# Optimization experiments

Measured on AMD Instinct MI355X. Metric: run time of the kernel, lower is better.

Reference implementation:

```python
import jax, jax.numpy as jnp
import numpy as np
from jax import lax

B, C_IN, H, W = 16, 2048, 16, 16
HIDDEN, N_ANC = 512, 9
N_POS, N_NEG = 2048, 2048
TOT = B * N_ANC * H * W  # 36864 = flat conf logits; also rows of reg.view(-1,4)


def _xyxy_to_cxcywh(b):
    x1, y1, x2, y2 = b[..., 0], b[..., 1], b[..., 2], b[..., 3]
    return jnp.stack([(x1 + x2) * 0.5, (y1 + y2) * 0.5, x2 - x1, y2 - y1], axis=-1)


def _cxcywh_to_xyxy(b):
    cx, cy, w, h = b[..., 0], b[..., 1], b[..., 2], b[..., 3]
    return jnp.stack([cx - w * 0.5, cy - h * 0.5, cx + w * 0.5, cy + h * 0.5], axis=-1)


def _rand_boxes(key, n):
    # valid xyxy boxes on the 16x16 feature-map coordinate grid, w,h in [1,4]
    k1, k2 = jax.random.split(key)
    xy = jax.random.uniform(k1, (n, 2), jnp.float32) * 12.0
    wh = 1.0 + jax.random.uniform(k2, (n, 2), jnp.float32) * 3.0
    return jnp.concatenate([xy, xy + wh], axis=-1)


def setup_inputs() -> dict:
    key = jax.random.key(0)
    ks = jax.random.split(key, 10)
    feature_map = jax.random.normal(ks[0], (B, C_IN, H, W), jnp.float32)
    pos_anc_ind = jax.random.randint(ks[1], (N_POS,), 0, TOT)
    neg_anc_ind = jax.random.randint(ks[2], (N_NEG,), 0, TOT)
    pos_anc_coords = _rand_boxes(ks[3], N_POS)
    gt_bboxes_pos = _rand_boxes(ks[4], N_POS)
    s1 = 1.0 / np.sqrt(C_IN * 9)
    W1 = jax.random.uniform(ks[5], (HIDDEN, C_IN, 3, 3), jnp.float32, -s1, s1)
    b1 = jnp.zeros((HIDDEN,), jnp.float32)
    s2 = 1.0 / np.sqrt(HIDDEN)
    Wc = jax.random.uniform(ks[6], (N_ANC, HIDDEN), jnp.float32, -s2, s2)
    bc = jnp.zeros((N_ANC,), jnp.float32)
    Wr = jax.random.uniform(ks[7], (N_ANC * 4, HIDDEN), jnp.float32, -s2, s2)
    br = jnp.zeros((N_ANC * 4,), jnp.float32)
    return {"feature_map": feature_map, "pos_anc_coords": pos_anc_coords,
            "gt_bboxes_pos": gt_bboxes_pos, "W1": W1, "b1": b1, "Wc": Wc,
            "bc": bc, "Wr": Wr, "br": br,
            "pos_anc_ind": pos_anc_ind, "neg_anc_ind": neg_anc_ind}


def generate_proposals(anchors, offsets):
    a = _xyxy_to_cxcywh(anchors)
    p = jnp.stack([a[:, 0] + offsets[:, 0] * a[:, 2],
                   a[:, 1] + offsets[:, 1] * a[:, 3],
                   a[:, 2] * jnp.exp(offsets[:, 2]),
                   a[:, 3] * jnp.exp(offsets[:, 3])], axis=-1)
    return _cxcywh_to_xyxy(p)


def calc_gt_offsets(anc, gt):
    a = _xyxy_to_cxcywh(anc)
    g = _xyxy_to_cxcywh(gt)
    tx = (g[:, 0] - a[:, 0]) / a[:, 2]
    ty = (g[:, 1] - a[:, 1]) / a[:, 3]
    tw = jnp.log(g[:, 2] / a[:, 2])
    th = jnp.log(g[:, 3] / a[:, 3])
    return jnp.stack([tx, ty, tw, th], axis=-1)


def reference(feature_map, pos_anc_coords, gt_bboxes_pos, W1, b1, Wc, bc, Wr, br,
              pos_anc_ind, neg_anc_ind):
    # ProposalModule: conv3x3 -> (dropout=identity in eval) -> relu -> 1x1 heads
    out = lax.conv_general_dilated(feature_map, W1, (1, 1), 'SAME',
                                   dimension_numbers=('NCHW', 'OIHW', 'NCHW'))
    out = jax.nn.relu(out + b1[None, :, None, None])
    conf = jnp.einsum('bchw,oc->bohw', out, Wc) + bc[None, :, None, None]   # [B,9,H,W]
    reg = jnp.einsum('bchw,oc->bohw', out, Wr) + br[None, :, None, None]    # [B,36,H,W]
    # irregular flat gathers, exactly mirroring torch .flatten()/.view(-1,4)
    conf_pos = conf.reshape(-1)[pos_anc_ind]
    conf_neg = conf.reshape(-1)[neg_anc_ind]
    offsets_pos = reg.reshape(-1, 4)[pos_anc_ind]
    proposals = generate_proposals(pos_anc_coords, offsets_pos)
    gt_offsets = calc_gt_offsets(pos_anc_coords, gt_bboxes_pos)
    # BCE-with-logits, targets 1 for pos / 0 for neg, reduction='sum' / B
    cls_loss = (jnp.sum(jax.nn.softplus(-conf_pos)) + jnp.sum(jax.nn.softplus(conf_neg))) / B
    # smooth L1 (beta=1), reduction='sum' / B
    d = offsets_pos - gt_offsets
    ad = jnp.abs(d)
    reg_loss = jnp.sum(jnp.where(ad < 1.0, 0.5 * d * d, ad - 0.5)) / B
    total_rpn_loss = 1.0 * cls_loss + 5.0 * reg_loss  # w_conf=1, w_reg=5
    return total_rpn_loss, proposals
```

## Files before the change

kernel.cpp:

```cpp
#include <hip/hip_runtime.h>
#include <hip/hip_bf16.h>
#include <stdint.h>

#define CIN 2048
#define HID 512
#define NPOS 2048
#define NNEG 2048

#define BM 256
#define BN 256
#define BK 64
#define NS 8
#define A_ELEMS (BM * BK)
#define B_ELEMS (BN * BK)

typedef __attribute__((ext_vector_type(8))) short s16x8;
typedef __attribute__((ext_vector_type(4))) short s16x4;
typedef __attribute__((ext_vector_type(4))) float f32x4;
typedef unsigned short ushort_t;

static __device__ __forceinline__ float bf2f(unsigned short u) {
    union { float f; unsigned int i; } v; v.i = ((unsigned int)u) << 16; return v.f;
}
static __device__ __forceinline__ unsigned short f2bf(float f) {
    union { float f; unsigned int i; } v; v.f = f;
    unsigned int r = v.i + 0x7FFF + ((v.i >> 16) & 1);
    return (unsigned short)(r >> 16);
}

typedef __attribute__((address_space(1))) const void gvoid_t;
typedef __attribute__((address_space(3))) void lvoid_t;
static __device__ __forceinline__ void gload16(const void* g, void* l) {
    __builtin_amdgcn_global_load_lds((gvoid_t*)g, (lvoid_t*)l, 16, 0, 0);
}

__global__ __launch_bounds__(256) void k_prep(const float* __restrict__ F,
                                              const float* __restrict__ W1,
                                              const float* __restrict__ Wc,
                                              const float* __restrict__ Wr,
                                              ushort_t* __restrict__ Fp,
                                              ushort_t* __restrict__ Wt2,
                                              ushort_t* __restrict__ Whp) {
    __shared__ float tile[128][17];
    __shared__ float buf[512 * 9];
    int bid = blockIdx.x;
    int t = threadIdx.x;
    if (bid < 1024) {
        int b = bid >> 6, rem = bid & 63;
        int y = rem >> 2, icq = rem & 3;
        for (int it = 0; it < 4; ++it) {
            int ic0 = icq * 512 + it * 128;
#pragma unroll
            for (int i2 = 0; i2 < 2; ++i2) {
                int idx = i2 * 256 + t;
                int ci = idx >> 2, xg = idx & 3;
                const float4 v = *(const float4*)&F[((size_t)(b * CIN + ic0 + ci) * 16 + y) * 16 + xg * 4];
                tile[ci][xg * 4 + 0] = v.x;
                tile[ci][xg * 4 + 1] = v.y;
                tile[ci][xg * 4 + 2] = v.z;
                tile[ci][xg * 4 + 3] = v.w;
            }
            __syncthreads();
#pragma unroll
            for (int i2 = 0; i2 < 2; ++i2) {
                int idx = i2 * 256 + t;
                int x = idx >> 5, cig = idx & 31;
                s16x4 o;
#pragma unroll
                for (int j = 0; j < 4; ++j) o[j] = (short)f2bf(tile[cig * 4 + j][x]);
                *(s16x4*)&Fp[((size_t)(b * 18 + y + 1) * 18 + (x + 1)) * CIN + ic0 + cig * 4] = o;
            }
            __syncthreads();
        }
    } else if (bid < 1536) {
        int oc = bid - 1024;
        for (int ic0 = 0; ic0 < CIN; ic0 += 512) {
            const float* src = W1 + ((size_t)oc * CIN + ic0) * 9;
            {
                const float4* s4 = (const float4*)src;
                float4* b4 = (float4*)buf;
                for (int i = t; i < 1152; i += 256) b4[i] = s4[i];
            }
            __syncthreads();
            for (int s = t; s < 9 * 64; s += 256) {
                int k = s >> 6, g = s & 63;
                s16x8 v;
#pragma unroll
                for (int j = 0; j < 8; ++j) v[j] = (short)f2bf(buf[(g * 8 + j) * 9 + k]);
                *(s16x8*)&Wt2[((size_t)(k * HID + oc)) * CIN + ic0 + g * 8] = v;
            }
            __syncthreads();
        }
    } else if (bid < 1600) {
        const s16x8 z = {0, 0, 0, 0, 0, 0, 0, 0};
        for (int idx = (bid - 1536) * 256 + t; idx < 16 * 68 * 256; idx += 64 * 256) {
            int seg = idx & 255;
            int cell = (idx >> 8) % 68;
            int b = idx / (68 * 256);
            int Y, X;
            if (cell < 18)      { Y = 0;         X = cell; }
            else if (cell < 36) { Y = 17;        X = cell - 18; }
            else if (cell < 52) { Y = cell - 35; X = 0; }
            else                { Y = cell - 51; X = 17; }
            *(s16x8*)&Fp[((size_t)(b * 18 + Y) * 18 + X) * CIN + seg * 8] = z;
        }
    } else {
#pragma unroll
        for (int i = 0; i < 12; ++i) {
            int sid = i * 256 + t;
            int o = sid >> 6, sg = sid & 63;
            s16x8 v;
#pragma unroll
            for (int j = 0; j < 8; ++j) {
                float w = 0.f;
                if (o < 9) w = Wc[o * HID + sg * 8 + j];
                else if (o < 45) w = Wr[(size_t)(o - 9) * HID + sg * 8 + j];
                v[j] = (short)f2bf(w);
            }
            *(s16x8*)&Whp[o * HID + ((sg ^ (o & 7)) << 3)] = v;
        }
    }
}

__global__ __launch_bounds__(512, 2) void k_gemm(const ushort_t* __restrict__ Fp,
                                                 const ushort_t* __restrict__ Wt2,
                                                 ushort_t* __restrict__ Part,
                                                 int icLen, int nPairs) {
    extern __shared__ ushort_t ldsbuf[];
    ushort_t* As = ldsbuf;
    ushort_t* Bs = ldsbuf + 3 * A_ELEMS;

    int bid = blockIdx.x;
    int rb = bid / nPairs;
    int pair = bid - rb * nPairs;
    int split = pair >> 1, cb = pair & 1;
    int icBase = split * icLen;
    int m0 = rb * BM, oc0 = cb * BN;
    int t = threadIdx.x;
    int wid = t >> 6, lane = t & 63;
    int wr = wid >> 2, wn = wid & 3;
    int hi = lane >> 4, lo = lane & 15;

    f32x4 acc[8][4];
#pragma unroll
    for (int a = 0; a < 8; ++a)
#pragma unroll
        for (int b = 0; b < 4; ++b) acc[a][b] = (f32x4){0.f, 0.f, 0.f, 0.f};

    int Abase[4], Bbase[4];
#pragma unroll
    for (int j = 0; j < 4; ++j) {
        int li = j * 512 + t;
        int row = li >> 3;
        int sg = (li & 7) ^ (row & 7);
        int m = m0 + row;
        int b = m >> 8, y = (m >> 4) & 15, x = m & 15;
        Abase[j] = ((b * 18 + y) * 18 + x) * CIN + sg * 8;
        Bbase[j] = (oc0 + row) * CIN + sg * 8;
    }
    int aidx[8][2], bidx[4][2];
#pragma unroll
    for (int fm = 0; fm < 8; ++fm)
#pragma unroll
        for (int ks = 0; ks < 2; ++ks) {
            int r = wr * 128 + fm * 16 + lo;
            aidx[fm][ks] = r * BK + ((ks * 32 + hi * 8) ^ ((r & 7) << 3));
        }
#pragma unroll
    for (int fn = 0; fn < 4; ++fn)
#pragma unroll
        for (int ks = 0; ks < 2; ++ks) {
            int rB = wn * 64 + fn * 16 + lo;
            bidx[fn][ks] = rB * BK + ((ks * 32 + hi * 8) ^ ((rB & 7) << 3));
        }

    const int nsteps = (icLen / BK) * 9;

#define STAGE_A(BUF, S)                                                              \
    do {                                                                             \
        int kidx_ = (S) % 9, icc_ = (S) / 9;                                         \
        int ak_ = ((kidx_ / 3) * 18 + (kidx_ - 3 * (kidx_ / 3))) * CIN + icBase + icc_ * BK; \
        ushort_t* dA_ = As + (BUF) * A_ELEMS;                                        \
        _Pragma("unroll") for (int j_ = 0; j_ < 4; ++j_)                             \
            gload16(Fp + Abase[j_] + ak_, dA_ + (size_t)(j_ * 512 + t) * 8);         \
    } while (0)
#define STAGE_B(BUF, S)                                                              \
    do {                                                                             \
        int kidx_ = (S) % 9, icc_ = (S) / 9;                                         \
        int bk_ = kidx_ * HID * CIN + icBase + icc_ * BK;                            \
        ushort_t* dB_ = Bs + (BUF) * B_ELEMS;                                        \
        _Pragma("unroll") for (int j_ = 0; j_ < 4; ++j_)                             \
            gload16(Wt2 + Bbase[j_] + bk_, dB_ + (size_t)(j_ * 512 + t) * 8);        \
    } while (0)

    STAGE_A(0, 0); STAGE_B(0, 0); STAGE_A(1, 1);
    asm volatile("s_waitcnt vmcnt(4)" ::: "memory");
    __builtin_amdgcn_s_barrier();
    __builtin_amdgcn_sched_barrier(0);

#pragma unroll 1
    for (int step = 0; step < nsteps; ++step) {
        const ushort_t* cA = As + (step % 3) * A_ELEMS;
        const ushort_t* cB = Bs + (step & 1) * B_ELEMS;
        if (step + 1 < nsteps) STAGE_B((step + 1) & 1, step + 1);
        s16x8 af[8][2], bf[4][2];
#pragma unroll
        for (int ks = 0; ks < 2; ++ks) {
#pragma unroll
            for (int fm = 0; fm < 8; ++fm) af[fm][ks] = *(const s16x8*)&cA[aidx[fm][ks]];
#pragma unroll
            for (int fn = 0; fn < 4; ++fn) bf[fn][ks] = *(const s16x8*)&cB[bidx[fn][ks]];
        }
        if (step + 2 < nsteps) STAGE_A((step + 2) % 3, step + 2);
        __builtin_amdgcn_s_setprio(1);
#pragma unroll
        for (int fm = 0; fm < 8; ++fm)
#pragma unroll
            for (int fn = 0; fn < 4; ++fn)
#pragma unroll
                for (int ks = 0; ks < 2; ++ks)
                    acc[fm][fn] = __builtin_amdgcn_mfma_f32_16x16x32_bf16(
                        af[fm][ks], bf[fn][ks], acc[fm][fn], 0, 0, 0);
        __builtin_amdgcn_s_setprio(0);
        if (step + 2 < nsteps) {
            asm volatile("s_waitcnt vmcnt(4)" ::: "memory");
            __builtin_amdgcn_s_barrier();
            __builtin_amdgcn_sched_barrier(0);
        } else if (step + 1 < nsteps) {
            asm volatile("s_waitcnt vmcnt(0)" ::: "memory");
            __builtin_amdgcn_s_barrier();
            __builtin_amdgcn_sched_barrier(0);
        }
    }
#undef STAGE_A
#undef STAGE_B

#pragma unroll
    for (int fm = 0; fm < 8; ++fm)
#pragma unroll
        for (int fn = 0; fn < 4; ++fn)
#pragma unroll
            for (int r = 0; r < 4; ++r) {
                int gm = m0 + wr * 128 + fm * 16 + hi * 4 + r;
                int gn = oc0 + wn * 64 + fn * 16 + lo;
                Part[((size_t)split * 4096 + gm) * HID + gn] = f2bf(acc[fm][fn][r]);
            }
}

__global__ __launch_bounds__(256) void k_heads(const ushort_t* __restrict__ Part, int ns,
                                               const ushort_t* __restrict__ Whp,
                                               const float* __restrict__ b1,
                                               const float* __restrict__ bc,
                                               const float* __restrict__ br,
                                               float* __restrict__ conf,
                                               float* __restrict__ reg) {
    extern __shared__ ushort_t hsm[];
    ushort_t* Ah = hsm;
    ushort_t* Wh = hsm + 16 * HID;
    int t = threadIdx.x;
    int wid = t >> 6, lane = t & 63;
    int hi = lane >> 4, lo = lane & 15;
    int row0 = blockIdx.x * 16;

#pragma unroll
    for (int i = 0; i < 12; ++i)
        gload16(Whp + (size_t)(i * 256 + t) * 8, Wh + (size_t)(i * 256 + t) * 8);

#pragma unroll
    for (int i = 0; i < 4; ++i) {
        int pos = i * 256 + t;
        int r = pos >> 6, sg = pos & 63;
        float s[8];
#pragma unroll
        for (int j = 0; j < 8; ++j) s[j] = 0.f;
        for (int sp = 0; sp < ns; ++sp) {
            s16x8 v = *(const s16x8*)&Part[((size_t)sp * 4096 + row0 + r) * HID + sg * 8];
#pragma unroll
            for (int j = 0; j < 8; ++j) s[j] += bf2f((unsigned short)v[j]);
        }
        s16x8 o;
#pragma unroll
        for (int j = 0; j < 8; ++j) o[j] = (short)f2bf(fmaxf(s[j] + b1[sg * 8 + j], 0.f));
        *(s16x8*)&Ah[r * HID + ((sg ^ (r & 7)) << 3)] = o;
    }
    __syncthreads();
    if (wid != 0) return;

    f32x4 acc[3];
#pragma unroll
    for (int fn = 0; fn < 3; ++fn) acc[fn] = (f32x4){0.f, 0.f, 0.f, 0.f};
#pragma unroll 1
    for (int kf = 0; kf < 16; ++kf) {
        int rA = lo;
        s16x8 a_ = *(const s16x8*)&Ah[rA * HID + ((kf * 32 + hi * 8) ^ ((rA & 7) << 3))];
#pragma unroll
        for (int fn = 0; fn < 3; ++fn) {
            int rB = fn * 16 + lo;
            s16x8 b_ = *(const s16x8*)&Wh[rB * HID + ((kf * 32 + hi * 8) ^ ((rB & 7) << 3))];
            acc[fn] = __builtin_amdgcn_mfma_f32_16x16x32_bf16(a_, b_, acc[fn], 0, 0, 0);
        }
    }
#pragma unroll
    for (int fn = 0; fn < 3; ++fn)
#pragma unroll
        for (int r = 0; r < 4; ++r) {
            int gm = row0 + hi * 4 + r;
            int o = fn * 16 + lo;
            float v = acc[fn][r];
            if (o < 9) conf[gm * 9 + o] = v + bc[o];
            else if (o < 45) reg[gm * 36 + (o - 9)] = v + br[o - 9];
        }
}

static __device__ __forceinline__ float softplus(float x) {
    return log1pf(expf(-fabsf(x))) + fmaxf(x, 0.f);
}

__global__ __launch_bounds__(1024) void k_loss(const float* __restrict__ conf,
                                               const float* __restrict__ reg,
                                               const int* __restrict__ pos_ind,
                                               const int* __restrict__ neg_ind,
                                               const float* __restrict__ anc,
                                               const float* __restrict__ gt,
                                               float* __restrict__ out) {
    int t = threadIdx.x;
    float cls = 0.f, rloss = 0.f;
    for (int p = t; p < NPOS; p += 1024) {
        int ind = pos_ind[p];
        {
            int b = ind / 2304, r = ind % 2304;
            int c = r >> 8, r2 = r & 255;
            float cv = conf[(b * 256 + r2) * 9 + c];
            cls += softplus(-cv);
        }
        float off[4];
#pragma unroll
        for (int j = 0; j < 4; ++j) {
            int e = 4 * ind + j;
            int b = e / 9216, r = e % 9216;
            int c = r >> 8, r2 = r & 255;
            off[j] = reg[(b * 256 + r2) * 36 + c];
        }
        float ax1 = anc[4 * p], ay1 = anc[4 * p + 1], ax2 = anc[4 * p + 2], ay2 = anc[4 * p + 3];
        float acx = (ax1 + ax2) * 0.5f, acy = (ay1 + ay2) * 0.5f;
        float aw = ax2 - ax1, ah = ay2 - ay1;
        float pcx = acx + off[0] * aw, pcy = acy + off[1] * ah;
        float pw = aw * expf(off[2]), ph = ah * expf(off[3]);
        out[1 + 4 * p + 0] = pcx - pw * 0.5f;
        out[1 + 4 * p + 1] = pcy - ph * 0.5f;
        out[1 + 4 * p + 2] = pcx + pw * 0.5f;
        out[1 + 4 * p + 3] = pcy + ph * 0.5f;
        float gx1 = gt[4 * p], gy1 = gt[4 * p + 1], gx2 = gt[4 * p + 2], gy2 = gt[4 * p + 3];
        float gcx = (gx1 + gx2) * 0.5f, gcy = (gy1 + gy2) * 0.5f;
        float gw = gx2 - gx1, gh = gy2 - gy1;
        float tv[4];
        tv[0] = (gcx - acx) / aw;
        tv[1] = (gcy - acy) / ah;
        tv[2] = logf(gw / aw);
        tv[3] = logf(gh / ah);
#pragma unroll
        for (int j = 0; j < 4; ++j) {
            float d = off[j] - tv[j];
            float ad = fabsf(d);
            rloss += (ad < 1.f) ? 0.5f * d * d : ad - 0.5f;
        }
    }
    for (int q = t; q < NNEG; q += 1024) {
        int ind = neg_ind[q];
        int b = ind / 2304, r = ind % 2304;
        int c = r >> 8, r2 = r & 255;
        float cv = conf[(b * 256 + r2) * 9 + c];
        cls += softplus(cv);
    }
    __shared__ float s1[1024], s2[1024];
    s1[t] = cls;
    s2[t] = rloss;
    __syncthreads();
    for (int s = 512; s > 0; s >>= 1) {
        if (t < s) {
            s1[t] += s1[t + s];
            s2[t] += s2[t + s];
        }
        __syncthreads();
    }
    if (t == 0) out[0] = (s1[0] + 5.f * s2[0]) / 16.f;
}

extern "C" void kernel_launch(void* const* d_in, const int* in_sizes, int n_in,
                              void* d_out, int out_size, void* d_ws, size_t ws_size,
                              hipStream_t stream) {
    const float* F   = (const float*)d_in[0];
    const float* anc = (const float*)d_in[1];
    const float* gt  = (const float*)d_in[2];
    const float* W1  = (const float*)d_in[3];
    const float* b1  = (const float*)d_in[4];
    const float* Wc  = (const float*)d_in[5];
    const float* bc  = (const float*)d_in[6];
    const float* Wr  = (const float*)d_in[7];
    const float* br  = (const float*)d_in[8];
    const int* pos_ind = (const int*)d_in[9];
    const int* neg_ind = (const int*)d_in[10];
    float* out = (float*)d_out;

    char* ws = (char*)d_ws;
    const size_t FP_BYTES   = (size_t)16 * 18 * 18 * CIN * 2;
    const size_t WT_BYTES   = (size_t)9 * HID * CIN * 2;
    const size_t PART_ONE   = (size_t)4096 * HID * 2;
    const size_t CONF_BYTES = (size_t)4096 * 9 * 4;
    const size_t REG_BYTES  = (size_t)4096 * 36 * 4;

    int icLen = CIN / NS;

    ushort_t* Fp   = (ushort_t*)ws;
    ushort_t* Wt2  = (ushort_t*)(ws + FP_BYTES);
    ushort_t* Part = (ushort_t*)(ws + FP_BYTES + WT_BYTES);
    float* conf    = (float*)(ws + FP_BYTES + WT_BYTES + (size_t)NS * PART_ONE);
    float* reg     = (float*)(ws + FP_BYTES + WT_BYTES + (size_t)NS * PART_ONE + CONF_BYTES);
    ushort_t* Whp  = (ushort_t*)(ws + FP_BYTES + WT_BYTES + (size_t)NS * PART_ONE + CONF_BYTES + REG_BYTES);

    const int GEMM_LDS = (3 * A_ELEMS + 2 * B_ELEMS) * 2;
    hipFuncSetAttribute((const void*)k_gemm, hipFuncAttributeMaxDynamicSharedMemorySize, GEMM_LDS);
    const int HEADS_LDS = (16 + 48) * HID * 2;
    hipFuncSetAttribute((const void*)k_heads, hipFuncAttributeMaxDynamicSharedMemorySize, HEADS_LDS);

    k_prep<<<1601, 256, 0, stream>>>(F, W1, Wc, Wr, Fp, Wt2, Whp);
    k_gemm<<<(4096 / BM) * (HID / BN) * NS, 512, GEMM_LDS, stream>>>(Fp, Wt2, Part, icLen, 2 * NS);
    k_heads<<<256, 256, HEADS_LDS, stream>>>(Part, NS, Whp, b1, bc, br, conf, reg);
    k_loss<<<1, 1024, 0, stream>>>(conf, reg, pos_ind, neg_ind, anc, gt, out);
}
```

Measured before the change: 125.4 us.

## Halve GEMM K-tile and register double-buffer LDS fragments in a ping-pong loop

The K tile of the implicit-GEMM conv drops from 64 to 32. LDS changes from 3 A buffers plus 2 B buffers to 2 of each, shrinking from 160KB to 64KB, and the swizzle is adjusted for the 4-segment rows. The main loop is rebuilt as a two-stage ping-pong: fragments for the next buffer are read into registers while the MFMAs run on the current ones, with one combined A+B stage per step and a full vmcnt/lgkmcnt(0) wait plus barrier after each step. This is meant to overlap LDS reads with MFMA work, but it doubles the number of barriers per unit of K, removes the partial vmcnt overlap the old code had, and raises register pressure by holding two fragment sets.

Result: slower. 132.7 us (+5.8%).

```diff
diff --git a/kernel.cpp b/kernel.cpp
--- a/kernel.cpp
+++ b/kernel.cpp
@@ -9,7 +9,7 @@
 
 #define BM 256
 #define BN 256
-#define BK 64
+#define BK 32
 #define NS 8
 #define A_ELEMS (BM * BK)
 #define B_ELEMS (BN * BK)
@@ -128,7 +128,7 @@
                                                  int icLen, int nPairs) {
     extern __shared__ ushort_t ldsbuf[];
     ushort_t* As = ldsbuf;
-    ushort_t* Bs = ldsbuf + 3 * A_ELEMS;
+    ushort_t* Bs = ldsbuf + 2 * A_ELEMS;
 
     int bid = blockIdx.x;
     int rb = bid / nPairs;
@@ -147,93 +147,92 @@
 #pragma unroll
         for (int b = 0; b < 4; ++b) acc[a][b] = (f32x4){0.f, 0.f, 0.f, 0.f};
 
-    int Abase[4], Bbase[4];
-#pragma unroll
-    for (int j = 0; j < 4; ++j) {
+    int Abase[2], Bbase[2];
+#pragma unroll
+    for (int j = 0; j < 2; ++j) {
         int li = j * 512 + t;
-        int row = li >> 3;
-        int sg = (li & 7) ^ (row & 7);
+        int row = li >> 2;
+        int sg = (li & 3) ^ ((row >> 1) & 3);
         int m = m0 + row;
         int b = m >> 8, y = (m >> 4) & 15, x = m & 15;
         Abase[j] = ((b * 18 + y) * 18 + x) * CIN + sg * 8;
         Bbase[j] = (oc0 + row) * CIN + sg * 8;
     }
-    int aidx[8][2], bidx[4][2];
-#pragma unroll
-    for (int fm = 0; fm < 8; ++fm)
-#pragma unroll
-        for (int ks = 0; ks < 2; ++ks) {
-            int r = wr * 128 + fm * 16 + lo;
-            aidx[fm][ks] = r * BK + ((ks * 32 + hi * 8) ^ ((r & 7) << 3));
-        }
-#pragma unroll
-    for (int fn = 0; fn < 4; ++fn)
-#pragma unroll
-        for (int ks = 0; ks < 2; ++ks) {
-            int rB = wn * 64 + fn * 16 + lo;
-            bidx[fn][ks] = rB * BK + ((ks * 32 + hi * 8) ^ ((rB & 7) << 3));
-        }
+    int aidx[8], bidx[4];
+#pragma unroll
+    for (int fm = 0; fm < 8; ++fm) {
+        int r = wr * 128 + fm * 16 + lo;
+        aidx[fm] = r * BK + ((hi ^ ((r >> 1) & 3)) << 3);
+    }
+#pragma unroll
+    for (int fn = 0; fn < 4; ++fn) {
+        int rB = wn * 64 + fn * 16 + lo;
+        bidx[fn] = rB * BK + ((hi ^ ((rB >> 1) & 3)) << 3);
+    }
 
     const int nsteps = (icLen / BK) * 9;
 
-#define STAGE_A(BUF, S)                                                              \
+#define STAGE(BUF, S)                                                                \
     do {                                                                             \
         int kidx_ = (S) % 9, icc_ = (S) / 9;                                         \
         int ak_ = ((kidx_ / 3) * 18 + (kidx_ - 3 * (kidx_ / 3))) * CIN + icBase + icc_ * BK; \
+        int bk_ = kidx_ * HID * CIN + icBase + icc_ * BK;                            \
         ushort_t* dA_ = As + (BUF) * A_ELEMS;                                        \
-        _Pragma("unroll") for (int j_ = 0; j_ < 4; ++j_)                             \
+        ushort_t* dB_ = Bs + (BUF) * B_ELEMS;                                        \
+        _Pragma("unroll") for (int j_ = 0; j_ < 2; ++j_) {                           \
             gload16(Fp + Abase[j_] + ak_, dA_ + (size_t)(j_ * 512 + t) * 8);         \
+            gload16(Wt2 + Bbase[j_] + bk_, dB_ + (size_t)(j_ * 512 + t) * 8);        \
+        }                                                                            \
     } while (0)
-#define STAGE_B(BUF, S)                                                              \
+
+#define READ_FRAGS(AV, BV, BUF)                                                      \
     do {                                                                             \
-        int kidx_ = (S) % 9, icc_ = (S) / 9;                                         \
-        int bk_ = kidx_ * HID * CIN + icBase + icc_ * BK;                            \
-        ushort_t* dB_ = Bs + (BUF) * B_ELEMS;                                        \
-        _Pragma("unroll") for (int j_ = 0; j_ < 4; ++j_)                             \
-            gload16(Wt2 + Bbase[j_] + bk_, dB_ + (size_t)(j_ * 512 + t) * 8);        \
+        const ushort_t* rA_ = As + (BUF) * A_ELEMS;                                  \
+        const ushort_t* rB_ = Bs + (BUF) * B_ELEMS;                                  \
+        _Pragma("unroll") for (int fm_ = 0; fm_ < 8; ++fm_) AV[fm_] = *(const s16x8*)&rA_[aidx[fm_]]; \
+        _Pragma("unroll") for (int fn_ = 0; fn_ < 4; ++fn_) BV[fn_] = *(const s16x8*)&rB_[bidx[fn_]]; \
     } while (0)
 
-    STAGE_A(0, 0); STAGE_B(0, 0); STAGE_A(1, 1);
-    asm volatile("s_waitcnt vmcnt(4)" ::: "memory");
-    __builtin_amdgcn_s_barrier();
-    __builtin_amdgcn_sched_barrier(0);
+#define MFMA_STEP(AV, BV)                                                            \
+    do {                                                                             \
+        __builtin_amdgcn_s_setprio(1);                                               \
+        _Pragma("unroll") for (int fm_ = 0; fm_ < 8; ++fm_)                          \
+            _Pragma("unroll") for (int fn_ = 0; fn_ < 4; ++fn_)                      \
+                acc[fm_][fn_] = __builtin_amdgcn_mfma_f32_16x16x32_bf16(             \
+                    AV[fm_], BV[fn_], acc[fm_][fn_], 0, 0, 0);                       \
+        __builtin_amdgcn_s_setprio(0);                                               \
+    } while (0)
+
+#define ENDSTEP()                                                                    \
+    do {                                                                             \
+        asm volatile("s_waitcnt vmcnt(0) lgkmcnt(0)" ::: "memory");                  \
+        __builtin_amdgcn_s_barrier();                                                \
+        __builtin_amdgcn_sched_barrier(0);                                           \
+    } while (0)
+
+    s16x8 a0[8], b0[4], a1[8], b1[4];
+
+    STAGE(0, 0);
+    ENDSTEP();
+    READ_FRAGS(a0, b0, 0);
+    STAGE(1, 1);
+    ENDSTEP();
 
 #pragma unroll 1
-    for (int step = 0; step < nsteps; ++step) {
-        const ushort_t* cA = As + (step % 3) * A_ELEMS;
-        const ushort_t* cB = Bs + (step & 1) * B_ELEMS;
-        if (step + 1 < nsteps) STAGE_B((step + 1) & 1, step + 1);
-        s16x8 af[8][2], bf[4][2];
-#pragma unroll
-        for (int ks = 0; ks < 2; ++ks) {
-#pragma unroll
-            for (int fm = 0; fm < 8; ++fm) af[fm][ks] = *(const s16x8*)&cA[aidx[fm][ks]];
-#pragma unroll
-            for (int fn = 0; fn < 4; ++fn) bf[fn][ks] = *(const s16x8*)&cB[bidx[fn][ks]];
-        }
-        if (step + 2 < nsteps) STAGE_A((step + 2) % 3, step + 2);
-        __builtin_amdgcn_s_setprio(1);
-#pragma unroll
-        for (int fm = 0; fm < 8; ++fm)
-#pragma unroll
-            for (int fn = 0; fn < 4; ++fn)
-#pragma unroll
-                for (int ks = 0; ks < 2; ++ks)
-                    acc[fm][fn] = __builtin_amdgcn_mfma_f32_16x16x32_bf16(
-                        af[fm][ks], bf[fn][ks], acc[fm][fn], 0, 0, 0);
-        __builtin_amdgcn_s_setprio(0);
-        if (step + 2 < nsteps) {
-            asm volatile("s_waitcnt vmcnt(4)" ::: "memory");
-            __builtin_amdgcn_s_barrier();
-            __builtin_amdgcn_sched_barrier(0);
-        } else if (step + 1 < nsteps) {
-            asm volatile("s_waitcnt vmcnt(0)" ::: "memory");
-            __builtin_amdgcn_s_barrier();
-            __builtin_amdgcn_sched_barrier(0);
-        }
-    }
-#undef STAGE_A
-#undef STAGE_B
+    for (int s = 0; s < nsteps; s += 2) {
+        if (s + 2 < nsteps) STAGE(0, s + 2);
+        READ_FRAGS(a1, b1, 1);
+        MFMA_STEP(a0, b0);
+        if (s + 2 < nsteps) ENDSTEP();
+        if (s + 3 < nsteps) STAGE(1, s + 3);
+        if (s + 2 < nsteps) READ_FRAGS(a0, b0, 0);
+        MFMA_STEP(a1, b1);
+        if (s + 3 < nsteps) ENDSTEP();
+    }
+#undef STAGE
+#undef READ_FRAGS
+#undef MFMA_STEP
+#undef ENDSTEP
 
 #pragma unroll
     for (int fm = 0; fm < 8; ++fm)
@@ -418,7 +417,7 @@
     float* reg     = (float*)(ws + FP_BYTES + WT_BYTES + (size_t)NS * PART_ONE + CONF_BYTES);
     ushort_t* Whp  = (ushort_t*)(ws + FP_BYTES + WT_BYTES + (size_t)NS * PART_ONE + CONF_BYTES + REG_BYTES);
 
-    const int GEMM_LDS = (3 * A_ELEMS + 2 * B_ELEMS) * 2;
+    const int GEMM_LDS = 2 * (A_ELEMS + B_ELEMS) * 2;
     hipFuncSetAttribute((const void*)k_gemm, hipFuncAttributeMaxDynamicSharedMemorySize, GEMM_LDS);
     const int HEADS_LDS = (16 + 48) * HID * 2;
     hipFuncSetAttribute((const void*)k_heads, hipFuncAttributeMaxDynamicSharedMemorySize, HEADS_LDS);
```
